# Optimization experiments

Measured on AMD Instinct MI355X. Metric: run time of the kernel, lower is better.

## Reference

```python
import jax, jax.numpy as jnp
import numpy as np

N_HEAD = 16

def setup_inputs() -> dict:
    key = jax.random.key(0)
    ks = jax.random.split(key, 5)
    B, T, D = 2, 2048, 1024
    k = D // N_HEAD
    scale = 0.02
    return {
        'x': jax.random.normal(ks[0], (B, T, D), dtype=jnp.float32),
        'Wq': jax.random.normal(ks[1], (D, D), dtype=jnp.float32) * scale,
        'Wk': jax.random.normal(ks[2], (D, k), dtype=jnp.float32) * scale,
        'Wv': jax.random.normal(ks[3], (D, k), dtype=jnp.float32) * scale,
        'Wo': jax.random.normal(ks[4], (D, D), dtype=jnp.float32) * scale,
    }

def reference(x, Wq, Wk, Wv, Wo):
    B, T, D = x.shape
    h = N_HEAD
    k = D // h
    Q = (x @ Wq).reshape(B, T, h, k)          # per-head queries
    K = x @ Wk                                 # single shared K head: (B,T,k)
    V = x @ Wv                                 # single shared V head: (B,T,k)
    scores = jnp.einsum('bthk,bsk->bhts', Q, K) / jnp.sqrt(jnp.float32(k))
    causal = jnp.tril(jnp.ones((T, T), dtype=bool))  # (T,T)
    scores = jnp.where(causal[None, None, :, :], scores, -jnp.inf)
    A = jax.nn.softmax(scores, axis=-1)        # (B,h,T,T)
    Y = jnp.einsum('bhts,bsk->bthk', A, V).reshape(B, T, D)
    return Y @ Wo
```

## Files before the change

### kernel.cpp

```cpp
#include <hip/hip_runtime.h>
#include <hip/hip_bf16.h>
#include <stdint.h>

typedef short short8 __attribute__((ext_vector_type(8)));
typedef float f32x4 __attribute__((ext_vector_type(4)));

constexpr int SEQ   = 2048;
constexpr int DM    = 1024;
constexpr int NHEAD = 16;
constexpr int HD    = 64;
constexpr int LDQ   = 1152;
constexpr int BATCH = 2;

__device__ __forceinline__ unsigned short f2bf(float f) {
    union { float f; uint32_t u; } v; v.f = f;
    uint32_t u = v.u;
    uint32_t r = (u + 0x7fffu + ((u >> 16) & 1u)) >> 16;
    return (unsigned short)r;
}

typedef __attribute__((address_space(1))) const void gvoid_t;
typedef __attribute__((address_space(3))) void lvoid_t;
__device__ __forceinline__ void gload16(const void* g, void* l) {
    __builtin_amdgcn_global_load_lds((gvoid_t*)g, (lvoid_t*)l, 16, 0, 0);
}

__global__ __launch_bounds__(256) void cast_x_kernel(
        const float* __restrict__ x, unsigned short* __restrict__ xb, int n) {
    int i = (blockIdx.x * 256 + threadIdx.x) * 4;
    if (i >= n) return;
    const float4 v = *(const float4*)(x + i);
    ushort4 o;
    o.x = f2bf(v.x); o.y = f2bf(v.y); o.z = f2bf(v.z); o.w = f2bf(v.w);
    *(ushort4*)(xb + i) = o;
}

__global__ __launch_bounds__(256) void prep_w_kernel(
        const float* __restrict__ Wq, const float* __restrict__ Wk,
        const float* __restrict__ Wv, const float* __restrict__ Wo,
        unsigned short* __restrict__ wtq, unsigned short* __restrict__ wot) {
    __shared__ unsigned short tile[32][33];
    int z = blockIdx.z;
    const float* W; unsigned short* Wt; int C;
    if (z == 0)      { W = Wq; Wt = wtq;                              C = DM; }
    else if (z == 1) { W = Wk; Wt = wtq + (size_t)DM * DM;            C = HD; }
    else if (z == 2) { W = Wv; Wt = wtq + (size_t)(DM + HD) * DM;     C = HD; }
    else             { W = Wo; Wt = wot;                              C = DM; }
    int c0 = blockIdx.x * 32, r0 = blockIdx.y * 32;
    if (c0 >= C) return;
    int tx = threadIdx.x & 31, ty = threadIdx.x >> 5;
    for (int i = ty; i < 32; i += 8)
        tile[i][tx] = f2bf(W[(size_t)(r0 + i) * C + (c0 + tx)]);
    __syncthreads();
    for (int i = ty; i < 32; i += 8)
        Wt[(size_t)(c0 + i) * DM + (r0 + tx)] = tile[tx][i];
}

__global__ __launch_bounds__(256) void gemm_kernel(
        const unsigned short* __restrict__ A,
        const unsigned short* __restrict__ Bt,
        void* __restrict__ Cout,
        unsigned short* __restrict__ VtOut,
        int M, int N, int K, int out_bf16, int ncols) {
    __shared__ unsigned short ldsA[3][128 * 64];
    __shared__ unsigned short ldsB[3][64 * 64];
    int lane = threadIdx.x & 63, wave = threadIdx.x >> 6;
    int ln = lane & 15, quad = lane >> 4;
    int wm = wave >> 1, wn = wave & 1;

    int g = blockIdx.x;
    int xcd = g & 7, idx = g >> 3;
    int rows_per_xcd = (int)(gridDim.x >> 3) / ncols;
    int row = xcd * rows_per_xcd + idx / ncols;
    int col = idx % ncols;
    int m0 = row * 128, n0 = col * 64;

    int t = threadIdx.x;
    int trow = t >> 3, tcb = t & 7;
    int gcb = tcb ^ (trow & 7);
    const unsigned short* gA = A + (size_t)(m0 + trow) * K + gcb * 8;
    const unsigned short* gB = Bt + (size_t)(n0 + trow) * K + gcb * 8;
    int dst = t * 8;

    auto stage = [&](int k0, int buf) {
#pragma unroll
        for (int rr = 0; rr < 4; ++rr)
            gload16(gA + (size_t)rr * 32 * K + k0, &ldsA[buf][dst + rr * 2048]);
#pragma unroll
        for (int rr = 0; rr < 2; ++rr)
            gload16(gB + (size_t)rr * 32 * K + k0, &ldsB[buf][dst + rr * 2048]);
    };

    f32x4 acc[4][2];
#pragma unroll
    for (int i = 0; i < 4; ++i)
#pragma unroll
        for (int j = 0; j < 2; ++j) acc[i][j] = f32x4{0, 0, 0, 0};

    int niter = K >> 6;
    stage(0, 0);
    stage(64, 1);
    for (int it = 0; it < niter; ++it) {
        if (it + 1 < niter)
            asm volatile("s_waitcnt vmcnt(6)" ::: "memory");
        else
            asm volatile("s_waitcnt vmcnt(0)" ::: "memory");
        __builtin_amdgcn_s_barrier();
        __builtin_amdgcn_sched_barrier(0);
        if (it + 2 < niter) stage((it + 2) << 6, (it + 2) % 3);
        const unsigned short* La = ldsA[it % 3];
        const unsigned short* Lb = ldsB[it % 3];
#pragma unroll
        for (int hh = 0; hh < 2; ++hh) {
            int kc = hh * 4 + quad;
            short8 aF[4], bF[2];
#pragma unroll
            for (int mt = 0; mt < 4; ++mt)
                aF[mt] = *(const short8*)&La[(wm * 64 + mt * 16 + ln) * 64 +
                                             ((kc ^ (ln & 7)) * 8)];
#pragma unroll
            for (int nt = 0; nt < 2; ++nt)
                bF[nt] = *(const short8*)&Lb[(wn * 32 + nt * 16 + ln) * 64 +
                                             ((kc ^ (ln & 7)) * 8)];
#pragma unroll
            for (int mt = 0; mt < 4; ++mt)
#pragma unroll
                for (int nt = 0; nt < 2; ++nt)
                    acc[mt][nt] = __builtin_amdgcn_mfma_f32_16x16x32_bf16(
                        aF[mt], bF[nt], acc[mt][nt], 0, 0, 0);
        }
    }

    if (out_bf16) {
        unsigned short* C = (unsigned short*)Cout;
#pragma unroll
        for (int mt = 0; mt < 4; ++mt)
#pragma unroll
            for (int nt = 0; nt < 2; ++nt)
#pragma unroll
                for (int r = 0; r < 4; ++r) {
                    int rr = m0 + wm * 64 + mt * 16 + quad * 4 + r;
                    int cc = n0 + wn * 32 + nt * 16 + ln;
                    unsigned short hv = f2bf(acc[mt][nt][r]);
                    C[(size_t)rr * N + cc] = hv;
                    if (VtOut != nullptr && cc >= DM + HD) {
                        int d = cc - (DM + HD);
                        int bb = rr >> 11, s = rr & 2047;
                        VtOut[((size_t)bb * HD + d) * SEQ + s] = hv;
                    }
                }
    } else {
        float* C = (float*)Cout;
#pragma unroll
        for (int mt = 0; mt < 4; ++mt)
#pragma unroll
            for (int nt = 0; nt < 2; ++nt)
#pragma unroll
                for (int r = 0; r < 4; ++r) {
                    int rr = m0 + wm * 64 + mt * 16 + quad * 4 + r;
                    int cc = n0 + wn * 32 + nt * 16 + ln;
                    C[(size_t)rr * N + cc] = acc[mt][nt][r];
                }
    }
}

__global__ __launch_bounds__(256) void attn_kernel(
        const unsigned short* __restrict__ QKV,
        const unsigned short* __restrict__ Vt,
        unsigned short* __restrict__ Y) {
    __shared__ unsigned short ldsK[2][64 * 64];
    __shared__ unsigned short ldsV[2][64 * 64];
    __shared__ unsigned short pbuf[4][16 * 64];

    int lane = threadIdx.x & 63, wave = threadIdx.x >> 6;
    int ln = lane & 15, quad = lane >> 4;
    int bid = blockIdx.x;
    int jg = 31 - (bid >> 5);
    int bh = bid & 31;
    int h = bh & 15, b = bh >> 4;
    int q0 = (jg * 4 + wave) * 16;
    const size_t baseRow = (size_t)b * SEQ;
    const unsigned short* Vb = Vt + (size_t)b * HD * SEQ;

    int t = threadIdx.x;
    int trow = t >> 3, tcb = t & 7;
    int cbg = tcb ^ (trow & 7);
    const unsigned short* gK = QKV + (baseRow + trow) * LDQ + DM + cbg * 8;
    const unsigned short* gV = Vb + (size_t)trow * SEQ + cbg * 8;
    int dstoff = trow * 64 + tcb * 8;

    auto stageKV = [&](int s0n, int buf) {
#pragma unroll
        for (int rr = 0; rr < 2; ++rr) {
            gload16(gK + (size_t)(s0n + 32 * rr) * LDQ, &ldsK[buf][dstoff + rr * 2048]);
            gload16(gV + (size_t)32 * rr * SEQ + s0n,   &ldsV[buf][dstoff + rr * 2048]);
        }
    };

    short8 aQ0, aQ1;
    {
        const unsigned short* qp = QKV + (baseRow + q0 + ln) * LDQ + h * HD + quad * 8;
        aQ0 = *(const short8*)(qp);
        aQ1 = *(const short8*)(qp + 32);
    }

    float lsum[4] = {0.f, 0.f, 0.f, 0.f};
    f32x4 o[4];
    for (int nt = 0; nt < 4; ++nt) o[nt] = f32x4{0, 0, 0, 0};

    const float c_exp = 0.1803368802f;
    unsigned short* pb = &pbuf[wave][0];

    auto computeStep = [&](int s0, int buf, bool partial) {
        const unsigned short* Kb = ldsK[buf];
        const unsigned short* Vf = ldsV[buf];
#pragma unroll
        for (int c = 0; c < 4; ++c) {
            int kbase = s0 + c * 16;
            if (partial && kbase > q0 + 15) {
#pragma unroll
                for (int r = 0; r < 4; ++r) {
                    int row = quad * 4 + r;
                    pb[row * 64 + (((c * 2 + (ln >> 3)) ^ (row & 7)) * 8) + (ln & 7)] = 0;
                }
                continue;
            }
            short8 k0f = *(const short8*)&Kb[(c * 16 + ln) * 64 + ((quad ^ (ln & 7)) * 8)];
            short8 k1f = *(const short8*)&Kb[(c * 16 + ln) * 64 + (((4 + quad) ^ (ln & 7)) * 8)];
            f32x4 s = {0, 0, 0, 0};
            s = __builtin_amdgcn_mfma_f32_16x16x32_bf16(aQ0, k0f, s, 0, 0, 0);
            s = __builtin_amdgcn_mfma_f32_16x16x32_bf16(aQ1, k1f, s, 0, 0, 0);
            bool diag = partial && (kbase + 15 > q0);
#pragma unroll
            for (int r = 0; r < 4; ++r) {
                float e = __builtin_exp2f(s[r] * c_exp);
                if (diag && (kbase + ln > q0 + quad * 4 + r)) e = 0.f;
                lsum[r] += e;
                int row = quad * 4 + r;
                pb[row * 64 + (((c * 2 + (ln >> 3)) ^ (row & 7)) * 8) + (ln & 7)] =
                    (unsigned short)(__float_as_uint(e) >> 16);
            }
        }
        short8 aP0 = *(const short8*)&pb[ln * 64 + ((quad ^ (ln & 7)) * 8)];
        short8 aP1 = *(const short8*)&pb[ln * 64 + (((4 + quad) ^ (ln & 7)) * 8)];
#pragma unroll
        for (int nt = 0; nt < 4; ++nt) {
            short8 v0 = *(const short8*)&Vf[(nt * 16 + ln) * 64 + ((quad ^ (ln & 7)) * 8)];
            short8 v1 = *(const short8*)&Vf[(nt * 16 + ln) * 64 + (((4 + quad) ^ (ln & 7)) * 8)];
            o[nt] = __builtin_amdgcn_mfma_f32_16x16x32_bf16(aP0, v0, o[nt], 0, 0, 0);
            o[nt] = __builtin_amdgcn_mfma_f32_16x16x32_bf16(aP1, v1, o[nt], 0, 0, 0);
        }
    };

    stageKV(0, 0);
    for (int it = 0; it < jg; ++it) {
        __syncthreads();
        stageKV((it + 1) * 64, (it + 1) & 1);
        computeStep(it * 64, it & 1, false);
    }
    __syncthreads();
    computeStep(jg * 64, jg & 1, true);

    for (int off = 1; off < 16; off <<= 1)
#pragma unroll
        for (int r = 0; r < 4; ++r) lsum[r] += __shfl_xor(lsum[r], off);
#pragma unroll
    for (int r = 0; r < 4; ++r) {
        float inv = 1.0f / lsum[r];
        int t_idx = q0 + quad * 4 + r;
        unsigned short* yp = Y + (baseRow + t_idx) * DM + h * HD + ln;
        for (int nt = 0; nt < 4; ++nt)
            yp[nt * 16] = f2bf(o[nt][r] * inv);
    }
}

extern "C" void kernel_launch(void* const* d_in, const int* in_sizes, int n_in,
                              void* d_out, int out_size, void* d_ws, size_t ws_size,
                              hipStream_t stream) {
    const float* x  = (const float*)d_in[0];
    const float* Wq = (const float*)d_in[1];
    const float* Wk = (const float*)d_in[2];
    const float* Wv = (const float*)d_in[3];
    const float* Wo = (const float*)d_in[4];
    float* out = (float*)d_out;

    char* ws = (char*)d_ws;
    unsigned short* xb  = (unsigned short*)(ws);
    unsigned short* y   = (unsigned short*)(ws);
    unsigned short* wtq = (unsigned short*)(ws + 8388608);
    unsigned short* wot = (unsigned short*)(ws + 10747904);
    unsigned short* qkv = (unsigned short*)(ws + 12845056);
    unsigned short* Vt  = (unsigned short*)(ws + 22282240);

    const int BT = BATCH * SEQ;

    hipLaunchKernelGGL(cast_x_kernel, dim3(BT * DM / 4 / 256), dim3(256), 0, stream,
                       x, xb, BT * DM);
    hipLaunchKernelGGL(prep_w_kernel, dim3(DM / 32, DM / 32, 4), dim3(256), 0, stream,
                       Wq, Wk, Wv, Wo, wtq, wot);

    hipLaunchKernelGGL(gemm_kernel, dim3((BT / 128) * (LDQ / 64)), dim3(256), 0, stream,
                       xb, wtq, (void*)qkv, Vt, BT, LDQ, DM, 1, LDQ / 64);

    hipLaunchKernelGGL(attn_kernel, dim3(32 * 32), dim3(256), 0, stream,
                       qkv, Vt, y);

    hipLaunchKernelGGL(gemm_kernel, dim3((BT / 128) * (DM / 64)), dim3(256), 0, stream,
                       y, wot, (void*)out, nullptr, BT, DM, DM, 0, DM / 64);
}
```

Before: 175.0 us.

## Software-pipeline attention QK/exp with PV and simplify GEMM to double buffering

The attention loop is split into QK+exp, P readback and PV phases. The next tile's QK^T and exp are computed while the current tile's PV product runs, and K and V staging are issued at separate points so each buffer is refilled as soon as it is free. This is meant to overlap transcendental and MFMA work and hide LDS and global latency across iterations. Separately, the GEMM goes from a three-stage LDS ring with a manual vmcnt wait to two-stage double buffering with __syncthreads, which saves LDS but may expose more load latency.

```diff
diff --git a/kernel.cpp b/kernel.cpp
--- a/kernel.cpp
+++ b/kernel.cpp
@@ -62,8 +62,8 @@
         void* __restrict__ Cout,
         unsigned short* __restrict__ VtOut,
         int M, int N, int K, int out_bf16, int ncols) {
-    __shared__ unsigned short ldsA[3][128 * 64];
-    __shared__ unsigned short ldsB[3][64 * 64];
+    __shared__ unsigned short ldsA[2][128 * 64];
+    __shared__ unsigned short ldsB[2][64 * 64];
     int lane = threadIdx.x & 63, wave = threadIdx.x >> 6;
     int ln = lane & 15, quad = lane >> 4;
     int wm = wave >> 1, wn = wave & 1;
@@ -97,19 +97,13 @@
 #pragma unroll
         for (int j = 0; j < 2; ++j) acc[i][j] = f32x4{0, 0, 0, 0};
 
+    stage(0, 0);
     int niter = K >> 6;
-    stage(0, 0);
-    stage(64, 1);
     for (int it = 0; it < niter; ++it) {
-        if (it + 1 < niter)
-            asm volatile("s_waitcnt vmcnt(6)" ::: "memory");
-        else
-            asm volatile("s_waitcnt vmcnt(0)" ::: "memory");
-        __builtin_amdgcn_s_barrier();
-        __builtin_amdgcn_sched_barrier(0);
-        if (it + 2 < niter) stage((it + 2) << 6, (it + 2) % 3);
-        const unsigned short* La = ldsA[it % 3];
-        const unsigned short* Lb = ldsB[it % 3];
+        __syncthreads();
+        if (it + 1 < niter) stage((it + 1) << 6, (it + 1) & 1);
+        const unsigned short* La = ldsA[it & 1];
+        const unsigned short* Lb = ldsB[it & 1];
 #pragma unroll
         for (int hh = 0; hh < 2; ++hh) {
             int kc = hh * 4 + quad;
@@ -189,12 +183,15 @@
     const unsigned short* gV = Vb + (size_t)trow * SEQ + cbg * 8;
     int dstoff = trow * 64 + tcb * 8;
 
-    auto stageKV = [&](int s0n, int buf) {
-#pragma unroll
-        for (int rr = 0; rr < 2; ++rr) {
+    auto stageK = [&](int s0n, int buf) {
+#pragma unroll
+        for (int rr = 0; rr < 2; ++rr)
             gload16(gK + (size_t)(s0n + 32 * rr) * LDQ, &ldsK[buf][dstoff + rr * 2048]);
-            gload16(gV + (size_t)32 * rr * SEQ + s0n,   &ldsV[buf][dstoff + rr * 2048]);
-        }
+    };
+    auto stageV = [&](int s0n, int buf) {
+#pragma unroll
+        for (int rr = 0; rr < 2; ++rr)
+            gload16(gV + (size_t)32 * rr * SEQ + s0n, &ldsV[buf][dstoff + rr * 2048]);
     };
 
     short8 aQ0, aQ1;
@@ -211,12 +208,11 @@
     const float c_exp = 0.1803368802f;
     unsigned short* pb = &pbuf[wave][0];
 
-    auto computeStep = [&](int s0, int buf, bool partial) {
+    auto QKexp = [&](int s, int buf, bool partial) {
         const unsigned short* Kb = ldsK[buf];
-        const unsigned short* Vf = ldsV[buf];
 #pragma unroll
         for (int c = 0; c < 4; ++c) {
-            int kbase = s0 + c * 16;
+            int kbase = s * 64 + c * 16;
             if (partial && kbase > q0 + 15) {
 #pragma unroll
                 for (int r = 0; r < 4; ++r) {
@@ -227,13 +223,13 @@
             }
             short8 k0f = *(const short8*)&Kb[(c * 16 + ln) * 64 + ((quad ^ (ln & 7)) * 8)];
             short8 k1f = *(const short8*)&Kb[(c * 16 + ln) * 64 + (((4 + quad) ^ (ln & 7)) * 8)];
-            f32x4 s = {0, 0, 0, 0};
-            s = __builtin_amdgcn_mfma_f32_16x16x32_bf16(aQ0, k0f, s, 0, 0, 0);
-            s = __builtin_amdgcn_mfma_f32_16x16x32_bf16(aQ1, k1f, s, 0, 0, 0);
+            f32x4 s2 = {0, 0, 0, 0};
+            s2 = __builtin_amdgcn_mfma_f32_16x16x32_bf16(aQ0, k0f, s2, 0, 0, 0);
+            s2 = __builtin_amdgcn_mfma_f32_16x16x32_bf16(aQ1, k1f, s2, 0, 0, 0);
             bool diag = partial && (kbase + 15 > q0);
 #pragma unroll
             for (int r = 0; r < 4; ++r) {
-                float e = __builtin_exp2f(s[r] * c_exp);
+                float e = __builtin_exp2f(s2[r] * c_exp);
                 if (diag && (kbase + ln > q0 + quad * 4 + r)) e = 0.f;
                 lsum[r] += e;
                 int row = quad * 4 + r;
@@ -241,8 +237,15 @@
                     (unsigned short)(__float_as_uint(e) >> 16);
             }
         }
-        short8 aP0 = *(const short8*)&pb[ln * 64 + ((quad ^ (ln & 7)) * 8)];
-        short8 aP1 = *(const short8*)&pb[ln * 64 + (((4 + quad) ^ (ln & 7)) * 8)];
+    };
+
+    auto readP = [&](short8& aP0, short8& aP1) {
+        aP0 = *(const short8*)&pb[ln * 64 + ((quad ^ (ln & 7)) * 8)];
+        aP1 = *(const short8*)&pb[ln * 64 + (((4 + quad) ^ (ln & 7)) * 8)];
+    };
+
+    auto PV = [&](int buf, short8 aP0, short8 aP1) {
+        const unsigned short* Vf = ldsV[buf];
 #pragma unroll
         for (int nt = 0; nt < 4; ++nt) {
             short8 v0 = *(const short8*)&Vf[(nt * 16 + ln) * 64 + ((quad ^ (ln & 7)) * 8)];
@@ -252,14 +255,24 @@
         }
     };
 
-    stageKV(0, 0);
+    stageK(0, 0); stageV(0, 0);
+    if (jg >= 1) { stageK(64, 1); stageV(64, 1); }
+    __syncthreads();
+    QKexp(0, 0, jg == 0);
+
     for (int it = 0; it < jg; ++it) {
         __syncthreads();
-        stageKV((it + 1) * 64, (it + 1) & 1);
-        computeStep(it * 64, it & 1, false);
-    }
-    __syncthreads();
-    computeStep(jg * 64, jg & 1, true);
+        if (it + 2 <= jg) stageK((it + 2) * 64, it & 1);
+        short8 aP0, aP1; readP(aP0, aP1);
+        QKexp(it + 1, (it + 1) & 1, (it + 1) == jg);
+        PV(it & 1, aP0, aP1);
+        __syncthreads();
+        if (it + 2 <= jg) stageV((it + 2) * 64, it & 1);
+    }
+    {
+        short8 aP0, aP1; readP(aP0, aP1);
+        PV(jg & 1, aP0, aP1);
+    }
 
     for (int off = 1; off < 16; off <<= 1)
 #pragma unroll
```

New measurement: 172.3 us. Within noise of the previous version (-1.5%).

## Replace LDS-staged GEMM with direct global-to-register MFMA operand loads

Applied to the files above, without the earlier changes.

The GEMM kernel no longer stages A and B tiles through a triple-buffered LDS pipeline with barriers. Each wave now loads its MFMA operand fragments straight from global memory into registers, double-buffered in registers across k-steps, with K fixed at compile time. This removes the LDS traffic and the workgroup barriers. In exchange, waves that share rows or columns re-read the same data from global/L2, and each lane's 16-byte loads are strided by row, so coalescing suffers.

```diff
diff --git a/kernel.cpp b/kernel.cpp
--- a/kernel.cpp
+++ b/kernel.cpp
@@ -11,6 +11,7 @@
 constexpr int HD    = 64;
 constexpr int LDQ   = 1152;
 constexpr int BATCH = 2;
+constexpr int KD    = 1024;
 
 __device__ __forceinline__ unsigned short f2bf(float f) {
     union { float f; uint32_t u; } v; v.f = f;
@@ -56,14 +57,12 @@
         Wt[(size_t)(c0 + i) * DM + (r0 + tx)] = tile[tx][i];
 }
 
-__global__ __launch_bounds__(256) void gemm_kernel(
+__global__ __launch_bounds__(256) void gemm_direct_kernel(
         const unsigned short* __restrict__ A,
         const unsigned short* __restrict__ Bt,
         void* __restrict__ Cout,
         unsigned short* __restrict__ VtOut,
-        int M, int N, int K, int out_bf16, int ncols) {
-    __shared__ unsigned short ldsA[3][128 * 64];
-    __shared__ unsigned short ldsB[3][64 * 64];
+        int N, int out_bf16, int ncols) {
     int lane = threadIdx.x & 63, wave = threadIdx.x >> 6;
     int ln = lane & 15, quad = lane >> 4;
     int wm = wave >> 1, wn = wave & 1;
@@ -75,21 +74,12 @@
     int col = idx % ncols;
     int m0 = row * 128, n0 = col * 64;
 
-    int t = threadIdx.x;
-    int trow = t >> 3, tcb = t & 7;
-    int gcb = tcb ^ (trow & 7);
-    const unsigned short* gA = A + (size_t)(m0 + trow) * K + gcb * 8;
-    const unsigned short* gB = Bt + (size_t)(n0 + trow) * K + gcb * 8;
-    int dst = t * 8;
-
-    auto stage = [&](int k0, int buf) {
-#pragma unroll
-        for (int rr = 0; rr < 4; ++rr)
-            gload16(gA + (size_t)rr * 32 * K + k0, &ldsA[buf][dst + rr * 2048]);
-#pragma unroll
-        for (int rr = 0; rr < 2; ++rr)
-            gload16(gB + (size_t)rr * 32 * K + k0, &ldsB[buf][dst + rr * 2048]);
-    };
+    const unsigned short* aB0 = A + (size_t)(m0 + wm * 64 +  0 + ln) * KD + quad * 8;
+    const unsigned short* aB1 = A + (size_t)(m0 + wm * 64 + 16 + ln) * KD + quad * 8;
+    const unsigned short* aB2 = A + (size_t)(m0 + wm * 64 + 32 + ln) * KD + quad * 8;
+    const unsigned short* aB3 = A + (size_t)(m0 + wm * 64 + 48 + ln) * KD + quad * 8;
+    const unsigned short* bB0 = Bt + (size_t)(n0 + wn * 32 +  0 + ln) * KD + quad * 8;
+    const unsigned short* bB1 = Bt + (size_t)(n0 + wn * 32 + 16 + ln) * KD + quad * 8;
 
     f32x4 acc[4][2];
 #pragma unroll
@@ -97,38 +87,33 @@
 #pragma unroll
         for (int j = 0; j < 2; ++j) acc[i][j] = f32x4{0, 0, 0, 0};
 
-    int niter = K >> 6;
-    stage(0, 0);
-    stage(64, 1);
-    for (int it = 0; it < niter; ++it) {
-        if (it + 1 < niter)
-            asm volatile("s_waitcnt vmcnt(6)" ::: "memory");
-        else
-            asm volatile("s_waitcnt vmcnt(0)" ::: "memory");
-        __builtin_amdgcn_s_barrier();
-        __builtin_amdgcn_sched_barrier(0);
-        if (it + 2 < niter) stage((it + 2) << 6, (it + 2) % 3);
-        const unsigned short* La = ldsA[it % 3];
-        const unsigned short* Lb = ldsB[it % 3];
-#pragma unroll
-        for (int hh = 0; hh < 2; ++hh) {
-            int kc = hh * 4 + quad;
-            short8 aF[4], bF[2];
-#pragma unroll
-            for (int mt = 0; mt < 4; ++mt)
-                aF[mt] = *(const short8*)&La[(wm * 64 + mt * 16 + ln) * 64 +
-                                             ((kc ^ (ln & 7)) * 8)];
-#pragma unroll
-            for (int nt = 0; nt < 2; ++nt)
-                bF[nt] = *(const short8*)&Lb[(wn * 32 + nt * 16 + ln) * 64 +
-                                             ((kc ^ (ln & 7)) * 8)];
-#pragma unroll
-            for (int mt = 0; mt < 4; ++mt)
-#pragma unroll
-                for (int nt = 0; nt < 2; ++nt)
-                    acc[mt][nt] = __builtin_amdgcn_mfma_f32_16x16x32_bf16(
-                        aF[mt], bF[nt], acc[mt][nt], 0, 0, 0);
-        }
+    short8 a0[4], b0[2], a1[4], b1[2];
+    a0[0] = *(const short8*)(aB0); a0[1] = *(const short8*)(aB1);
+    a0[2] = *(const short8*)(aB2); a0[3] = *(const short8*)(aB3);
+    b0[0] = *(const short8*)(bB0); b0[1] = *(const short8*)(bB1);
+
+#pragma unroll
+    for (int kk = 0; kk < KD; kk += 64) {
+        a1[0] = *(const short8*)(aB0 + kk + 32); a1[1] = *(const short8*)(aB1 + kk + 32);
+        a1[2] = *(const short8*)(aB2 + kk + 32); a1[3] = *(const short8*)(aB3 + kk + 32);
+        b1[0] = *(const short8*)(bB0 + kk + 32); b1[1] = *(const short8*)(bB1 + kk + 32);
+#pragma unroll
+        for (int mt = 0; mt < 4; ++mt)
+#pragma unroll
+            for (int nt = 0; nt < 2; ++nt)
+                acc[mt][nt] = __builtin_amdgcn_mfma_f32_16x16x32_bf16(
+                    a0[mt], b0[nt], acc[mt][nt], 0, 0, 0);
+        if (kk + 64 < KD) {
+            a0[0] = *(const short8*)(aB0 + kk + 64); a0[1] = *(const short8*)(aB1 + kk + 64);
+            a0[2] = *(const short8*)(aB2 + kk + 64); a0[3] = *(const short8*)(aB3 + kk + 64);
+            b0[0] = *(const short8*)(bB0 + kk + 64); b0[1] = *(const short8*)(bB1 + kk + 64);
+        }
+#pragma unroll
+        for (int mt = 0; mt < 4; ++mt)
+#pragma unroll
+            for (int nt = 0; nt < 2; ++nt)
+                acc[mt][nt] = __builtin_amdgcn_mfma_f32_16x16x32_bf16(
+                    a1[mt], b1[nt], acc[mt][nt], 0, 0, 0);
     }
 
     if (out_bf16) {
@@ -299,12 +284,12 @@
     hipLaunchKernelGGL(prep_w_kernel, dim3(DM / 32, DM / 32, 4), dim3(256), 0, stream,
                        Wq, Wk, Wv, Wo, wtq, wot);
 
-    hipLaunchKernelGGL(gemm_kernel, dim3((BT / 128) * (LDQ / 64)), dim3(256), 0, stream,
-                       xb, wtq, (void*)qkv, Vt, BT, LDQ, DM, 1, LDQ / 64);
+    hipLaunchKernelGGL(gemm_direct_kernel, dim3((BT / 128) * (LDQ / 64)), dim3(256), 0, stream,
+                       xb, wtq, (void*)qkv, Vt, LDQ, 1, LDQ / 64);
 
     hipLaunchKernelGGL(attn_kernel, dim3(32 * 32), dim3(256), 0, stream,
                        qkv, Vt, y);
 
-    hipLaunchKernelGGL(gemm_kernel, dim3((BT / 128) * (DM / 64)), dim3(256), 0, stream,
-                       y, wot, (void*)out, nullptr, BT, DM, DM, 0, DM / 64);
-}
+    hipLaunchKernelGGL(gemm_direct_kernel, dim3((BT / 128) * (DM / 64)), dim3(256), 0, stream,
+                       y, wot, (void*)out, nullptr, DM, 0, DM / 64);
+}
```

Result: slower. 243.1 us (+38.9%).
